# Optimization experiments

Hardware: AMD Instinct MI355X
Metric: run time of the kernel (lower is better)

The kernel has to match this reference:

```python
import jax, jax.numpy as jnp
import numpy as np

# Static multi-scale feature map shapes (H_l, W_l)
SHAPES = ((112, 112), (56, 56), (28, 28))
D_MODEL, D_HEAD, N_HEADS, N_LEVELS, N_POINTS = 256, 64, 6, 3, 9


def setup_inputs() -> dict:
    key = jax.random.key(0)
    ks = jax.random.split(key, 14)
    N, Lq = 4, 2048
    Lin = sum(h * w for h, w in SHAPES)  # 16464
    s = 0.02  # weight init scale
    return {
        "tgt": jax.random.normal(ks[0], (N, Lq, D_MODEL), jnp.float32),
        "src": jax.random.normal(ks[1], (N, Lin, D_MODEL), jnp.float32),
        "query_pos": jax.random.normal(ks[2], (N, Lq, D_MODEL), jnp.float32),
        "reference_points": jax.random.uniform(ks[3], (N, Lq, N_LEVELS, 2), jnp.float32),
        "src_spatial_shapes": jnp.array(SHAPES, jnp.int32),
        "level_start_index": jnp.array([0, 112 * 112, 112 * 112 + 56 * 56], jnp.int32),
        "src_padding_mask": jnp.zeros((N, Lin), bool),
        "W_off": jax.random.normal(ks[4], (D_MODEL, N_HEADS * N_LEVELS * N_POINTS * 2), jnp.float32) * s,
        "b_off": jax.random.normal(ks[5], (N_HEADS * N_LEVELS * N_POINTS * 2,), jnp.float32) * 0.5,
        "W_attn": jax.random.normal(ks[6], (D_MODEL, N_HEADS * N_LEVELS * N_POINTS), jnp.float32) * s,
        "b_attn": jax.random.normal(ks[7], (N_HEADS * N_LEVELS * N_POINTS,), jnp.float32) * s,
        "W_val": jax.random.normal(ks[8], (D_MODEL, N_HEADS * D_HEAD), jnp.float32) * s,
        "b_val": jnp.zeros((N_HEADS * D_HEAD,), jnp.float32),
        "W_out": jax.random.normal(ks[9], (N_HEADS * D_HEAD, D_MODEL), jnp.float32) * s,
        "b_out": jnp.zeros((D_MODEL,), jnp.float32),
    }


def _bilinear_sample(v, loc, H_l, W_l):
    """v: (N, Hh, H_l*W_l, d) level values; loc: (N, Lq, Hh, P, 2) in [0,1].
    grid_sample(align_corners=False, padding_mode='zeros') equivalent.
    Returns (N, Hh, Lq, P, d)."""
    N, Hh, _, d = v.shape
    Lq, P = loc.shape[1], loc.shape[3]
    x = loc[..., 0] * W_l - 0.5  # (N, Lq, Hh, P)
    y = loc[..., 1] * H_l - 0.5
    x0 = jnp.floor(x)
    y0 = jnp.floor(y)
    wx1 = x - x0
    wy1 = y - y0
    wx0 = 1.0 - wx1
    wy0 = 1.0 - wy1
    x0i = x0.astype(jnp.int32)
    y0i = y0.astype(jnp.int32)

    def gather(xi, yi, w):
        inb = (xi >= 0) & (xi < W_l) & (yi >= 0) & (yi < H_l)
        xc = jnp.clip(xi, 0, W_l - 1)
        yc = jnp.clip(yi, 0, H_l - 1)
        idx = (yc * W_l + xc).transpose(0, 2, 1, 3).reshape(N, Hh, Lq * P)
        g = jnp.take_along_axis(v, idx[..., None], axis=2)  # (N, Hh, Lq*P, d)
        w_eff = (w * inb).transpose(0, 2, 1, 3).reshape(N, Hh, Lq * P, 1)
        return g * w_eff

    out = (gather(x0i, y0i, wx0 * wy0)
           + gather(x0i + 1, y0i, wx1 * wy0)
           + gather(x0i, y0i + 1, wx0 * wy1)
           + gather(x0i + 1, y0i + 1, wx1 * wy1))
    return out.reshape(N, Hh, Lq, P, d)


def reference(tgt, src, query_pos, reference_points, src_spatial_shapes,
              level_start_index, src_padding_mask, W_off, b_off, W_attn, b_attn,
              W_val, b_val, W_out, b_out):
    N, Lq, _ = tgt.shape
    Hh, d, L, P = N_HEADS, D_HEAD, N_LEVELS, N_POINTS
    q = tgt + query_pos  # with_pos_embed

    value = src @ W_val + b_val
    value = jnp.where(src_padding_mask[..., None], 0.0, value)
    value = value.reshape(N, -1, Hh, d).transpose(0, 2, 1, 3)  # (N, Hh, Lin, d)

    off = (q @ W_off + b_off).reshape(N, Lq, Hh, L, P, 2)
    attn = jax.nn.softmax((q @ W_attn + b_attn).reshape(N, Lq, Hh, L * P), axis=-1)
    attn = attn.reshape(N, Lq, Hh, L, P)

    # offset_normalizer = (W_l, H_l); loc in normalized [0,1] coordinates
    norm = jnp.array([[w, h] for h, w in SHAPES], dtype=q.dtype)  # (L, 2)
    loc = reference_points[:, :, None, :, None, :] + off / norm[None, None, None, :, None, :]

    out = jnp.zeros((N, Hh, Lq, d), dtype=q.dtype)
    start = 0
    for l, (H_l, W_l) in enumerate(SHAPES):
        v_l = value[:, :, start:start + H_l * W_l]
        sampled = _bilinear_sample(v_l, loc[:, :, :, l], H_l, W_l)  # (N, Hh, Lq, P, d)
        out = out + jnp.einsum('nhqpd,nqhp->nhqd', sampled, attn[:, :, :, l])
        start += H_l * W_l

    out = out.transpose(0, 2, 1, 3).reshape(N, Lq, Hh * d)
    return out @ W_out + b_out  # dropout = identity in eval mode
```

## Files before the change

### kernel.cpp

```cpp
#include <hip/hip_runtime.h>
#include <math.h>

#define NB 4
#define LQ 2048
#define DM 256
#define HH 6
#define DH 64
#define LIN 16464
#define NOA 512
#define NVAL 384

typedef unsigned short ushort_t;
typedef unsigned int uint_t;
typedef __attribute__((ext_vector_type(8))) short s8v;
typedef __attribute__((ext_vector_type(4))) float f4v;

__device__ __forceinline__ ushort_t f2bf(float f) {
  union { float f; unsigned u; } v; v.f = f;
  unsigned r = v.u + 0x7fffu + ((v.u >> 16) & 1u);
  return (ushort_t)(r >> 16);
}

__device__ __forceinline__ uint_t cvtpk(float lo, float hi) {
  uint_t r;
  asm("v_cvt_pk_bf16_f32 %0, %1, %2" : "=v"(r) : "v"(lo), "v"(hi));
  return r;
}

typedef __attribute__((address_space(3))) char lds_char_t;
typedef const __attribute__((address_space(1))) char glb_char_t;
__device__ __forceinline__ void gload16(const void* g, void* l) {
  __builtin_amdgcn_global_load_lds((glb_char_t*)g, (lds_char_t*)l, 16, 0, 0);
}

__global__ __launch_bounds__(256)
void prep_k(const float4* __restrict__ tgt, const float4* __restrict__ qpos,
            ushort4* __restrict__ q_bf,
            const float* __restrict__ W_val, ushort_t* __restrict__ bt_val,
            const float* __restrict__ W_off, const float* __restrict__ W_attn,
            ushort_t* __restrict__ bt_oa,
            const float* __restrict__ W_out, ushort_t* __restrict__ bt_out,
            const float* __restrict__ b_off, const float* __restrict__ b_attn,
            float* __restrict__ bias_oa) {
  const int blk = blockIdx.x, tid = threadIdx.x;
  if (blk < 2048) {
    const int i = blk * 256 + tid;
    float4 x = tgt[i], y = qpos[i];
    ushort4 r;
    r.x = f2bf(x.x + y.x); r.y = f2bf(x.y + y.y);
    r.z = f2bf(x.z + y.z); r.w = f2bf(x.w + y.w);
    q_bf[i] = r;
  } else {
    const int i = (blk - 2048) * 256 + tid;
    if (i < 98304) {
      const int n = i >> 8, k = i & 255;
      bt_val[i] = f2bf(W_val[(size_t)k * 384 + n]);
    } else if (i < 229376) {
      const int j = i - 98304;
      const int n = j >> 8, k = j & 255;
      float v = 0.f;
      if (n < 324) v = W_off[(size_t)k * 324 + n];
      else if (n < 486) v = W_attn[(size_t)k * 162 + (n - 324)];
      bt_oa[j] = f2bf(v);
    } else if (i < 327680) {
      const int j = i - 229376;
      const int n = j / 384, k = j - n * 384;
      bt_out[j] = f2bf(W_out[(size_t)k * 256 + n]);
    } else {
      const int j = i - 327680;
      if (j < 512) bias_oa[j] = (j < 324) ? b_off[j] : (j < 486 ? b_attn[j - 324] : 0.f);
    }
  }
}

template <int CPX>
__global__ __launch_bounds__(256)
void mfma_gemm_vsrc_k(const float* __restrict__ Src, const ushort_t* __restrict__ Wt,
                      const float* __restrict__ bias, ushort_t* __restrict__ Cout) {
  __shared__ char lds[3][16384];
  const int bid = blockIdx.x;
  const int r = (bid & 7) * CPX + (bid >> 3);
  if (r >= 1548) return;
  const int bx = r / 3, by = r - bx * 3;
  const int bq = bx / 129;
  const int rb = (bx - bq * 129) * 128;
  const int n0 = by * 128;

  const int t = threadIdx.x;
  const int lane = t & 63, wid = t >> 6;
  const int wr = wid >> 1, wc = wid & 1;
  const int l15 = lane & 15, kg = lane >> 4;

  const int srow = lane >> 2;
  const int koct = (lane & 3) ^ ((lane >> 3) & 3);
  const int rsw = (l15 >> 1) & 3;
  const size_t WS0 = (size_t)(n0 + wid * 16 + srow) * DM + koct * 8;
  const size_t WS1 = WS0 + (size_t)64 * DM;

  const int ar = t >> 2, sA = t & 3;
  const int oA = sA ^ (((ar & 15) >> 1) & 3);
  const int rA0 = rb + ar, rA1 = rb + ar + 64;
  const float* pa = Src + ((size_t)bq * LIN + (rA0 < LIN ? rA0 : LIN - 1)) * DM + oA * 8;
  const float* pb = Src + ((size_t)bq * LIN + (rA1 < LIN ? rA1 : LIN - 1)) * DM + oA * 8;

  f4v acc[4][4];
#pragma unroll
  for (int i = 0; i < 4; ++i)
#pragma unroll
    for (int j = 0; j < 4; ++j) acc[i][j] = (f4v){0.f, 0.f, 0.f, 0.f};

  float4 lA[4], lB[4];

#define AL(dst_, g_)                                                     \
  { const int kb_ = (g_) << 5;                                           \
    dst_[0] = *(const float4*)(pa + kb_);                                \
    dst_[1] = *(const float4*)(pa + kb_ + 4);                            \
    dst_[2] = *(const float4*)(pb + kb_);                                \
    dst_[3] = *(const float4*)(pb + kb_ + 4); }

#define AW(src_, g_)                                                    \
  { char* d_ = &lds[(g_) % 3][8192] + t * 16;                           \
    uint4 c0, c1;                                                       \
    c0.x = cvtpk(src_[0].x, src_[0].y); c0.y = cvtpk(src_[0].z, src_[0].w); \
    c0.z = cvtpk(src_[1].x, src_[1].y); c0.w = cvtpk(src_[1].z, src_[1].w); \
    c1.x = cvtpk(src_[2].x, src_[2].y); c1.y = cvtpk(src_[2].z, src_[2].w); \
    c1.z = cvtpk(src_[3].x, src_[3].y); c1.w = cvtpk(src_[3].z, src_[3].w); \
    *(uint4*)(d_) = c0;                                                 \
    *(uint4*)(d_ + 4096) = c1; }

#define GW(g_)                                                          \
  { char* d_ = &lds[(g_) % 3][0]; const int ko_ = (g_) << 5;            \
    gload16(Wt + WS0 + ko_, d_ + wid * 1024);                           \
    gload16(Wt + WS1 + ko_, d_ + 4096 + wid * 1024); }

  AL(lA, 0);
  GW(0);
  asm volatile("s_waitcnt vmcnt(2)" ::: "memory");
  AW(lA, 0);
  AL(lA, 1);
  GW(1);
  asm volatile("s_waitcnt vmcnt(2)" ::: "memory");
  AW(lA, 1);
  AL(lA, 2);

#pragma unroll
  for (int gs = 0; gs < 8; ++gs) {
    if (gs <= 4) {
      if (gs & 1) { AL(lA, gs + 3); } else { AL(lB, gs + 3); }
    }
    if (gs == 7) asm volatile("s_waitcnt vmcnt(0)" ::: "memory");
    asm volatile("s_waitcnt lgkmcnt(0)" ::: "memory");
    __builtin_amdgcn_s_barrier();
    asm volatile("" ::: "memory");
    if (gs <= 5) GW(gs + 2);

    const char* d = &lds[gs % 3][0];
    s8v av[4], bv[4];
#pragma unroll
    for (int mr = 0; mr < 4; ++mr)
      av[mr] = *(const s8v*)(d + (wr * 64 + mr * 16 + l15) * 64 + ((kg ^ rsw) << 4));
#pragma unroll
    for (int nr = 0; nr < 4; ++nr)
      bv[nr] = *(const s8v*)(d + 8192 + (wc * 64 + nr * 16 + l15) * 64 + ((kg ^ rsw) << 4));
#pragma unroll
    for (int mr = 0; mr < 4; ++mr)
#pragma unroll
      for (int nr = 0; nr < 4; ++nr)
        acc[mr][nr] = __builtin_amdgcn_mfma_f32_16x16x32_bf16(av[mr], bv[nr],
                                                              acc[mr][nr], 0, 0, 0);

    if (gs <= 5) {
      if (gs <= 4) {
        asm volatile("s_waitcnt vmcnt(6)" ::: "memory");
      } else {
        asm volatile("s_waitcnt vmcnt(2)" ::: "memory");
      }
      if (gs & 1) { AW(lB, gs + 2); } else { AW(lA, gs + 2); }
    }
  }
#undef AL
#undef AW
#undef GW

#pragma unroll
  for (int mr = 0; mr < 4; ++mr) {
    const int ch = n0 + wr * 64 + mr * 16 + kg * 4;
    const int h = ch >> 6, dd = ch & 63;
    const float4 b4 = *(const float4*)(bias + ch);
    ushort_t* obase = Cout + (size_t)(bq * HH + h) * LIN * DH + dd;
#pragma unroll
    for (int nr = 0; nr < 4; ++nr) {
      const int ii = rb + wc * 64 + nr * 16 + l15;
      if (ii < LIN) {
        ushort4 o;
        o.x = f2bf(acc[mr][nr][0] + b4.x);
        o.y = f2bf(acc[mr][nr][1] + b4.y);
        o.z = f2bf(acc[mr][nr][2] + b4.z);
        o.w = f2bf(acc[mr][nr][3] + b4.w);
        *(ushort4*)(obase + (size_t)ii * DH) = o;
      }
    }
  }
}

template <int NBX, int NBY, int CPX>
__global__ __launch_bounds__(256)
void mfma_gemm_k(const ushort_t* __restrict__ Act, const ushort_t* __restrict__ Wt,
                 const float* __restrict__ bias, float* __restrict__ Cout,
                 int N, int K) {
  __shared__ char lds[3][16384];
  const int bid = blockIdx.x;
  const int r = (bid & 7) * CPX + (bid >> 3);
  if (r >= NBX * NBY) return;
  const int bx = r / NBY, by = r - bx * NBY;
  const int m0 = bx * 128, n0 = by * 128;

  const int t = threadIdx.x;
  const int lane = t & 63, wid = t >> 6;
  const int wr = wid >> 1, wc = wid & 1;
  const int l15 = lane & 15, kg = lane >> 4;
  const int nk = K >> 5;

  const int srow = lane >> 2;
  const int koct = (lane & 3) ^ ((lane >> 3) & 3);
  const int rsw = (l15 >> 1) & 3;

  const size_t WA0 = (size_t)(n0 + wid * 16 + srow) * K + koct * 8;
  const size_t WA1 = WA0 + (size_t)64 * K;
  const size_t XB0 = (size_t)(m0 + wid * 16 + srow) * K + koct * 8;
  const size_t XB1 = XB0 + (size_t)64 * K;

  f4v acc[4][4];
#pragma unroll
  for (int i = 0; i < 4; ++i)
#pragma unroll
    for (int j = 0; j < 4; ++j) acc[i][j] = (f4v){0.f, 0.f, 0.f, 0.f};

#define STAGE(ks_)                                                       \
  { char* d_ = &lds[(ks_) % 3][0]; const int ko_ = (ks_) << 5;           \
    gload16(Wt + WA0 + ko_,  d_ + wid * 1024);                           \
    gload16(Wt + WA1 + ko_,  d_ + 4096 + wid * 1024);                    \
    gload16(Act + XB0 + ko_, d_ + 8192 + wid * 1024);                    \
    gload16(Act + XB1 + ko_, d_ + 12288 + wid * 1024); }

  STAGE(0);
  STAGE(1);

  for (int ks = 0; ks < nk; ++ks) {
    if (ks + 1 < nk) {
      asm volatile("s_waitcnt vmcnt(4)" ::: "memory");
    } else {
      asm volatile("s_waitcnt vmcnt(0)" ::: "memory");
    }
    __builtin_amdgcn_s_barrier();
    asm volatile("" ::: "memory");
    if (ks + 2 < nk) STAGE(ks + 2);

    const char* d = &lds[ks % 3][0];
    s8v av[4], bv[4];
#pragma unroll
    for (int mr = 0; mr < 4; ++mr)
      av[mr] = *(const s8v*)(d + (wr * 64 + mr * 16 + l15) * 64 + ((kg ^ rsw) << 4));
#pragma unroll
    for (int nr = 0; nr < 4; ++nr)
      bv[nr] = *(const s8v*)(d + 8192 + (wc * 64 + nr * 16 + l15) * 64 + ((kg ^ rsw) << 4));
#pragma unroll
    for (int mr = 0; mr < 4; ++mr)
#pragma unroll
      for (int nr = 0; nr < 4; ++nr)
        acc[mr][nr] = __builtin_amdgcn_mfma_f32_16x16x32_bf16(av[mr], bv[nr],
                                                              acc[mr][nr], 0, 0, 0);
  }
#undef STAGE

#pragma unroll
  for (int mr = 0; mr < 4; ++mr) {
    const int ch = n0 + wr * 64 + mr * 16 + kg * 4;
    const float4 b4 = *(const float4*)(bias + ch);
#pragma unroll
    for (int nr = 0; nr < 4; ++nr) {
      const int qrow = m0 + wc * 64 + nr * 16 + l15;
      float4 v;
      v.x = acc[mr][nr][0] + b4.x;
      v.y = acc[mr][nr][1] + b4.y;
      v.z = acc[mr][nr][2] + b4.z;
      v.w = acc[mr][nr][3] + b4.w;
      *(float4*)(Cout + (size_t)qrow * N + ch) = v;
    }
  }
}

__global__ __launch_bounds__(256)
void deform_sample_k(const ushort_t* __restrict__ value,
                     const float* __restrict__ oa,
                     const float* __restrict__ refp,
                     uint_t* __restrict__ otmp) {
  __shared__ int4 sp[4][56];
  const int lane = threadIdx.x & 63, wv = threadIdx.x >> 6;
  const int wid = blockIdx.x * 4 + wv;
  const int s = wid >> 11;
  const int qq = wid & 2047;
  const int nb = s / HH, h = s - nb * HH;
  const int nq = nb * LQ + qq;

  float lg = -INFINITY;
  if (lane < 27) lg = oa[(size_t)nq * NOA + 324 + h * 27 + lane];
  float mx = lg;
#pragma unroll
  for (int m = 1; m < 64; m <<= 1) mx = fmaxf(mx, __shfl_xor(mx, m, 64));
  float e = (lane < 27) ? __expf(lg - mx) : 0.f;
  float ssum = e;
#pragma unroll
  for (int m = 1; m < 64; m <<= 1) ssum += __shfl_xor(ssum, m, 64);

  if (lane < 27) {
    const float aw = e / ssum;
    const int lvl = (lane >= 18) ? 2 : (lane >= 9 ? 1 : 0);
    const float Wf = (lvl == 0) ? 112.f : (lvl == 1 ? 56.f : 28.f);
    const int Wi = (lvl == 0) ? 112 : (lvl == 1 ? 56 : 28);
    const int base = (lvl == 0) ? 0 : (lvl == 1 ? 12544 : 15680);
    const float2 rp = *(const float2*)(refp + (size_t)nq * 6 + lvl * 2);
    const float2 of = *(const float2*)(oa + (size_t)nq * NOA + h * 54 + lane * 2);
    const float x = rp.x * Wf + of.x - 0.5f;
    const float y = rp.y * Wf + of.y - 0.5f;
    const float x0f = floorf(x), y0f = floorf(y);
    const float wx1 = x - x0f, wy1 = y - y0f;
    const float wx0 = 1.f - wx1, wy0 = 1.f - wy1;
    const int x0 = (int)x0f, y0 = (int)y0f;
    const int x1 = x0 + 1, y1 = y0 + 1;
    const bool bx0 = (x0 >= 0) & (x0 < Wi), bx1 = (x1 >= 0) & (x1 < Wi);
    const bool by0 = (y0 >= 0) & (y0 < Wi), by1 = (y1 >= 0) & (y1 < Wi);
    const int a00 = (bx0 & by0) ? ((base + y0 * Wi + x0) << 7) : 0;
    const int a01 = (bx1 & by0) ? ((base + y0 * Wi + x1) << 7) : 0;
    const int a10 = (bx0 & by1) ? ((base + y1 * Wi + x0) << 7) : 0;
    const int a11 = (bx1 & by1) ? ((base + y1 * Wi + x1) << 7) : 0;
    const float w00 = (bx0 & by0) ? aw * wx0 * wy0 : 0.f;
    const float w01 = (bx1 & by0) ? aw * wx1 * wy0 : 0.f;
    const float w10 = (bx0 & by1) ? aw * wx0 * wy1 : 0.f;
    const float w11 = (bx1 & by1) ? aw * wx1 * wy1 : 0.f;
    sp[wv][lane * 2 + 0] = make_int4(a00, __float_as_int(w00), a01, __float_as_int(w01));
    sp[wv][lane * 2 + 1] = make_int4(a10, __float_as_int(w10), a11, __float_as_int(w11));
  } else if (lane == 27) {
    sp[wv][54] = make_int4(0, 0, 0, 0);
    sp[wv][55] = make_int4(0, 0, 0, 0);
  }
  __syncthreads();

  const uint_t slice = (uint_t)__builtin_amdgcn_readfirstlane(s);
  const char* vbase = (const char*)value + (size_t)slice * (LIN * DH * 2);
  const int j4 = (lane & 31) * 4;
  const int half = lane >> 5;
  float a0 = 0.f, a1 = 0.f;
#pragma unroll 2
  for (int i = 0; i < 14; ++i) {
    const int pt = half * 14 + i;
    const int4 c01 = sp[wv][pt * 2];
    const int4 c23 = sp[wv][pt * 2 + 1];
    const uint_t u0 = *(const uint_t*)(vbase + (uint_t)(c01.x + j4));
    const uint_t u1 = *(const uint_t*)(vbase + (uint_t)(c01.z + j4));
    const uint_t u2 = *(const uint_t*)(vbase + (uint_t)(c23.x + j4));
    const uint_t u3 = *(const uint_t*)(vbase + (uint_t)(c23.z + j4));
    const float w0 = __int_as_float(c01.y), w1 = __int_as_float(c01.w);
    const float w2 = __int_as_float(c23.y), w3 = __int_as_float(c23.w);
    a0 += w0 * __uint_as_float(u0 << 16);
    a1 += w0 * __uint_as_float(u0 & 0xffff0000u);
    a0 += w1 * __uint_as_float(u1 << 16);
    a1 += w1 * __uint_as_float(u1 & 0xffff0000u);
    a0 += w2 * __uint_as_float(u2 << 16);
    a1 += w2 * __uint_as_float(u2 & 0xffff0000u);
    a0 += w3 * __uint_as_float(u3 << 16);
    a1 += w3 * __uint_as_float(u3 & 0xffff0000u);
  }
  a0 += __shfl_xor(a0, 32, 64);
  a1 += __shfl_xor(a1, 32, 64);
  if (lane < 32) {
    const uint_t packed = (uint_t)f2bf(a0) | ((uint_t)f2bf(a1) << 16);
    otmp[(size_t)nq * 192 + h * 32 + lane] = packed;
  }
}

extern "C" void kernel_launch(void* const* d_in, const int* in_sizes, int n_in,
                              void* d_out, int out_size, void* d_ws, size_t ws_size,
                              hipStream_t stream) {
  const float* tgt   = (const float*)d_in[0];
  const float* src   = (const float*)d_in[1];
  const float* qpos  = (const float*)d_in[2];
  const float* refp  = (const float*)d_in[3];
  const float* W_off  = (const float*)d_in[7];
  const float* b_off  = (const float*)d_in[8];
  const float* W_attn = (const float*)d_in[9];
  const float* b_attn = (const float*)d_in[10];
  const float* W_val  = (const float*)d_in[11];
  const float* b_val  = (const float*)d_in[12];
  const float* W_out  = (const float*)d_in[13];
  const float* b_out  = (const float*)d_in[14];

  char* ws = (char*)d_ws;
  ushort_t* val_bf  = (ushort_t*)(ws);
  float*    oa      = (float*)   (ws + 50577408);
  ushort_t* q_bf    = (ushort_t*)(ws + 67354624);
  uint_t*   otmp    = (uint_t*)  (ws + 71548928);
  ushort_t* bt_val  = (ushort_t*)(ws + 77840384);
  ushort_t* bt_oa   = (ushort_t*)(ws + 78036992);
  ushort_t* bt_out  = (ushort_t*)(ws + 78299136);
  float*    bias_oa = (float*)   (ws + 78495744);

  prep_k<<<3330, 256, 0, stream>>>((const float4*)tgt, (const float4*)qpos,
                                   (ushort4*)q_bf, W_val, bt_val,
                                   W_off, W_attn, bt_oa, W_out, bt_out,
                                   b_off, b_attn, bias_oa);

  mfma_gemm_vsrc_k<194><<<1552, 256, 0, stream>>>(src, bt_val, b_val, val_bf);
  mfma_gemm_k<64, 4, 32><<<256, 256, 0, stream>>>(
      q_bf, bt_oa, bias_oa, oa, NOA, DM);

  deform_sample_k<<<12288, 256, 0, stream>>>(val_bf, oa, refp, otmp);

  mfma_gemm_k<64, 2, 16><<<128, 256, 0, stream>>>(
      (const ushort_t*)otmp, bt_out, b_out, (float*)d_out, DM, NVAL);
}
```

Before: 109.7 us.

## Keep full src row tile in LDS and loop over all value-projection column blocks

The value projection GEMM now has each block load its 128-row fp32 src tile once, convert it to bf16 and keep the whole K=256 slab in LDS (64 KB). It then iterates over the three 128-column output blocks, streaming weight slices through a double buffer. Before, three blocks re-read and re-converted the same src rows. This cuts the grid from 1548 to 516 blocks and raises LDS use to 80 KB per block, which lowers occupancy and parallelism. The src load phase is also no longer overlapped with MFMA work.

```diff
diff --git a/kernel.cpp b/kernel.cpp
--- a/kernel.cpp
+++ b/kernel.cpp
@@ -77,14 +77,12 @@
 __global__ __launch_bounds__(256)
 void mfma_gemm_vsrc_k(const float* __restrict__ Src, const ushort_t* __restrict__ Wt,
                       const float* __restrict__ bias, ushort_t* __restrict__ Cout) {
-  __shared__ char lds[3][16384];
+  __shared__ char lds[81920];
   const int bid = blockIdx.x;
   const int r = (bid & 7) * CPX + (bid >> 3);
-  if (r >= 1548) return;
-  const int bx = r / 3, by = r - bx * 3;
-  const int bq = bx / 129;
-  const int rb = (bx - bq * 129) * 128;
-  const int n0 = by * 128;
+  if (r >= 516) return;
+  const int bq = r / 129;
+  const int rb = (r - bq * 129) * 128;
 
   const int t = threadIdx.x;
   const int lane = t & 63, wid = t >> 6;
@@ -94,8 +92,7 @@
   const int srow = lane >> 2;
   const int koct = (lane & 3) ^ ((lane >> 3) & 3);
   const int rsw = (l15 >> 1) & 3;
-  const size_t WS0 = (size_t)(n0 + wid * 16 + srow) * DM + koct * 8;
-  const size_t WS1 = WS0 + (size_t)64 * DM;
+  const size_t WSb = (size_t)(wid * 16 + srow) * DM + koct * 8;
 
   const int ar = t >> 2, sA = t & 3;
   const int oA = sA ^ (((ar & 15) >> 1) & 3);
@@ -110,6 +107,7 @@
     for (int j = 0; j < 4; ++j) acc[i][j] = (f4v){0.f, 0.f, 0.f, 0.f};
 
   float4 lA[4], lB[4];
+  uint4 wA0, wA1, wB0, wB1;
 
 #define AL(dst_, g_)                                                     \
   { const int kb_ = (g_) << 5;                                           \
@@ -119,7 +117,7 @@
     dst_[3] = *(const float4*)(pb + kb_ + 4); }
 
 #define AW(src_, g_)                                                    \
-  { char* d_ = &lds[(g_) % 3][8192] + t * 16;                           \
+  { char* d_ = &lds[(g_) * 8192] + t * 16;                              \
     uint4 c0, c1;                                                       \
     c0.x = cvtpk(src_[0].x, src_[0].y); c0.y = cvtpk(src_[0].z, src_[0].w); \
     c0.z = cvtpk(src_[1].x, src_[1].y); c0.w = cvtpk(src_[1].z, src_[1].w); \
@@ -128,79 +126,113 @@
     *(uint4*)(d_) = c0;                                                 \
     *(uint4*)(d_ + 4096) = c1; }
 
-#define GW(g_)                                                          \
-  { char* d_ = &lds[(g_) % 3][0]; const int ko_ = (g_) << 5;            \
-    gload16(Wt + WS0 + ko_, d_ + wid * 1024);                           \
-    gload16(Wt + WS1 + ko_, d_ + 4096 + wid * 1024); }
+#define WL(a_, b_, s_)                                                  \
+  { const size_t o_ = WSb + (size_t)((s_) >> 3) * 32768 + (((s_) & 7) << 5); \
+    a_ = *(const uint4*)(Wt + o_);                                      \
+    b_ = *(const uint4*)(Wt + o_ + (size_t)64 * DM); }
+
+#define WW(a_, b_, s_)                                                  \
+  { char* d_ = &lds[65536 + (((s_) & 1) << 13)] + wid * 1024 + lane * 16; \
+    *(uint4*)(d_) = a_;                                                 \
+    *(uint4*)(d_ + 4096) = b_; }
+
+#define FLUSH(by_)                                                      \
+  {                                                                     \
+    _Pragma("unroll")                                                   \
+    for (int mr = 0; mr < 4; ++mr) {                                    \
+      const int ch = (by_) * 128 + wr * 64 + mr * 16 + kg * 4;          \
+      const int h = ch >> 6, dd = ch & 63;                              \
+      const float4 b4 = *(const float4*)(bias + ch);                    \
+      ushort_t* obase = Cout + (size_t)(bq * HH + h) * LIN * DH + dd;   \
+      _Pragma("unroll")                                                 \
+      for (int nr = 0; nr < 4; ++nr) {                                  \
+        const int ii = rb + wc * 64 + nr * 16 + l15;                    \
+        if (ii < LIN) {                                                 \
+          ushort4 o;                                                    \
+          o.x = f2bf(acc[mr][nr][0] + b4.x);                            \
+          o.y = f2bf(acc[mr][nr][1] + b4.y);                            \
+          o.z = f2bf(acc[mr][nr][2] + b4.z);                            \
+          o.w = f2bf(acc[mr][nr][3] + b4.w);                            \
+          *(ushort4*)(obase + (size_t)ii * DH) = o;                     \
+        }                                                               \
+      }                                                                 \
+    }                                                                   \
+  }
 
   AL(lA, 0);
-  GW(0);
+  AL(lB, 1);
+#pragma unroll
+  for (int g = 0; g < 8; ++g) {
+    if (g < 7) {
+      asm volatile("s_waitcnt vmcnt(4)" ::: "memory");
+    } else {
+      asm volatile("s_waitcnt vmcnt(0)" ::: "memory");
+    }
+    if (g & 1) { AW(lB, g); } else { AW(lA, g); }
+    if (g + 2 < 8) {
+      if (g & 1) { AL(lB, g + 2); } else { AL(lA, g + 2); }
+    }
+  }
+
+  WL(wA0, wA1, 0);
+  WL(wB0, wB1, 1);
   asm volatile("s_waitcnt vmcnt(2)" ::: "memory");
-  AW(lA, 0);
-  AL(lA, 1);
-  GW(1);
-  asm volatile("s_waitcnt vmcnt(2)" ::: "memory");
-  AW(lA, 1);
-  AL(lA, 2);
-
-#pragma unroll
-  for (int gs = 0; gs < 8; ++gs) {
-    if (gs <= 4) {
-      if (gs & 1) { AL(lA, gs + 3); } else { AL(lB, gs + 3); }
-    }
-    if (gs == 7) asm volatile("s_waitcnt vmcnt(0)" ::: "memory");
-    asm volatile("s_waitcnt lgkmcnt(0)" ::: "memory");
-    __builtin_amdgcn_s_barrier();
-    asm volatile("" ::: "memory");
-    if (gs <= 5) GW(gs + 2);
-
-    const char* d = &lds[gs % 3][0];
-    s8v av[4], bv[4];
-#pragma unroll
-    for (int mr = 0; mr < 4; ++mr)
-      av[mr] = *(const s8v*)(d + (wr * 64 + mr * 16 + l15) * 64 + ((kg ^ rsw) << 4));
-#pragma unroll
-    for (int nr = 0; nr < 4; ++nr)
-      bv[nr] = *(const s8v*)(d + 8192 + (wc * 64 + nr * 16 + l15) * 64 + ((kg ^ rsw) << 4));
-#pragma unroll
-    for (int mr = 0; mr < 4; ++mr)
+  WW(wA0, wA1, 0);
+  asm volatile("s_waitcnt lgkmcnt(0)" ::: "memory");
+  __builtin_amdgcn_s_barrier();
+  asm volatile("" ::: "memory");
+
+#pragma unroll
+  for (int by = 0; by < 3; ++by) {
+#pragma unroll
+    for (int k = 0; k < 8; ++k) {
+      const int s = by * 8 + k;
+      if (s + 2 < 24) {
+        if (s & 1) { WL(wB0, wB1, s + 2); } else { WL(wA0, wA1, s + 2); }
+      }
+      const char* dw = &lds[65536 + ((s & 1) << 13)];
+      const char* da = &lds[k * 8192];
+      s8v av[4], bv[4];
+#pragma unroll
+      for (int mr = 0; mr < 4; ++mr)
+        av[mr] = *(const s8v*)(dw + (wr * 64 + mr * 16 + l15) * 64 + ((kg ^ rsw) << 4));
 #pragma unroll
       for (int nr = 0; nr < 4; ++nr)
-        acc[mr][nr] = __builtin_amdgcn_mfma_f32_16x16x32_bf16(av[mr], bv[nr],
-                                                              acc[mr][nr], 0, 0, 0);
-
-    if (gs <= 5) {
-      if (gs <= 4) {
-        asm volatile("s_waitcnt vmcnt(6)" ::: "memory");
-      } else {
-        asm volatile("s_waitcnt vmcnt(2)" ::: "memory");
+        bv[nr] = *(const s8v*)(da + (wc * 64 + nr * 16 + l15) * 64 + ((kg ^ rsw) << 4));
+#pragma unroll
+      for (int mr = 0; mr < 4; ++mr)
+#pragma unroll
+        for (int nr = 0; nr < 4; ++nr)
+          acc[mr][nr] = __builtin_amdgcn_mfma_f32_16x16x32_bf16(av[mr], bv[nr],
+                                                                acc[mr][nr], 0, 0, 0);
+
+      if (s + 1 < 24) {
+        if (s + 2 < 24) {
+          asm volatile("s_waitcnt vmcnt(2)" ::: "memory");
+        } else {
+          asm volatile("s_waitcnt vmcnt(0)" ::: "memory");
+        }
+        if (s & 1) { WW(wA0, wA1, s + 1); } else { WW(wB0, wB1, s + 1); }
+        asm volatile("s_waitcnt lgkmcnt(0)" ::: "memory");
+        __builtin_amdgcn_s_barrier();
+        asm volatile("" ::: "memory");
       }
-      if (gs & 1) { AW(lB, gs + 2); } else { AW(lA, gs + 2); }
+      if (k == 7) {
+        FLUSH(by);
+        if (by < 2) {
+#pragma unroll
+          for (int i = 0; i < 4; ++i)
+#pragma unroll
+            for (int j = 0; j < 4; ++j) acc[i][j] = (f4v){0.f, 0.f, 0.f, 0.f};
+        }
+      }
     }
   }
 #undef AL
 #undef AW
-#undef GW
-
-#pragma unroll
-  for (int mr = 0; mr < 4; ++mr) {
-    const int ch = n0 + wr * 64 + mr * 16 + kg * 4;
-    const int h = ch >> 6, dd = ch & 63;
-    const float4 b4 = *(const float4*)(bias + ch);
-    ushort_t* obase = Cout + (size_t)(bq * HH + h) * LIN * DH + dd;
-#pragma unroll
-    for (int nr = 0; nr < 4; ++nr) {
-      const int ii = rb + wc * 64 + nr * 16 + l15;
-      if (ii < LIN) {
-        ushort4 o;
-        o.x = f2bf(acc[mr][nr][0] + b4.x);
-        o.y = f2bf(acc[mr][nr][1] + b4.y);
-        o.z = f2bf(acc[mr][nr][2] + b4.z);
-        o.w = f2bf(acc[mr][nr][3] + b4.w);
-        *(ushort4*)(obase + (size_t)ii * DH) = o;
-      }
-    }
-  }
+#undef WL
+#undef WW
+#undef FLUSH
 }
 
 template <int NBX, int NBY, int CPX>
@@ -410,7 +442,7 @@
                                    W_off, W_attn, bt_oa, W_out, bt_out,
                                    b_off, b_attn, bias_oa);
 
-  mfma_gemm_vsrc_k<194><<<1552, 256, 0, stream>>>(src, bt_val, b_val, val_bf);
+  mfma_gemm_vsrc_k<65><<<520, 256, 0, stream>>>(src, bt_val, b_val, val_bf);
   mfma_gemm_k<64, 4, 32><<<256, 256, 0, stream>>>(
       q_bf, bt_oa, bias_oa, oa, NOA, DM);
 
```

After: 115.3 us. +5.1%, slower.
